# Performance work log

Measured on AMD Instinct MI355X. Metric: run time of the kernel, lower is better.

## Reference

```python
import jax, jax.numpy as jnp
import numpy as np

N_NODES = 50000
N_EDGES = 600000
IN_DIM = 128
HID = 64
HEADS = 4
NEG_SLOPE = 0.2


def _glorot(key, shape):
    fan_in, fan_out = shape[0], shape[-1]
    lim = jnp.sqrt(6.0 / (fan_in + fan_out))
    return jax.random.uniform(key, shape, jnp.float32, -lim, lim)


def setup_inputs() -> dict:
    key = jax.random.key(0)
    ks = jax.random.split(key, 16)
    x = jax.random.normal(ks[0], (N_NODES, IN_DIM), jnp.float32)
    edge_index = jax.random.randint(ks[1], (2, N_EDGES), 0, N_NODES, jnp.int32)
    # GAT layer 1: in=128 -> heads=4, out=64, concat -> 256
    W1 = _glorot(ks[2], (IN_DIM, HEADS * HID))
    a_src1 = _glorot(ks[3], (HEADS, HID))
    a_dst1 = _glorot(ks[4], (HEADS, HID))
    b1 = jnp.zeros((HEADS * HID,), jnp.float32)
    # GAT layer 2: in=256 -> heads=1, out=64, no concat
    W2 = _glorot(ks[5], (HEADS * HID, 1 * HID))
    a_src2 = _glorot(ks[6], (1, HID))
    a_dst2 = _glorot(ks[7], (1, HID))
    b2 = jnp.zeros((HID,), jnp.float32)
    # classifier: Linear(64,32) -> ReLU -> Dropout(eval: identity) -> Linear(32,2)
    Wc1 = _glorot(ks[8], (HID, 32))
    bc1 = jnp.zeros((32,), jnp.float32)
    Wc2 = _glorot(ks[9], (32, 2))
    bc2 = jnp.zeros((2,), jnp.float32)
    return {"x": x, "edge_index": edge_index,
            "W1": W1, "a_src1": a_src1, "a_dst1": a_dst1, "b1": b1,
            "W2": W2, "a_src2": a_src2, "a_dst2": a_dst2, "b2": b2,
            "Wc1": Wc1, "bc1": bc1, "Wc2": Wc2, "bc2": bc2}


def _gat_conv(x, src, dst, W, a_src, a_dst, b, heads, out_ch, concat):
    N = x.shape[0]
    h = (x @ W).reshape(N, heads, out_ch)          # [N,H,C]
    alpha_s = jnp.sum(h * a_src, axis=-1)          # [N,H]
    alpha_d = jnp.sum(h * a_dst, axis=-1)          # [N,H]
    e = jax.nn.leaky_relu(alpha_s[src] + alpha_d[dst], NEG_SLOPE)  # [E,H]
    # segment softmax over edges grouped by destination node
    m = jax.ops.segment_max(e, dst, num_segments=N)                # [N,H]
    ex = jnp.exp(e - m[dst])
    denom = jax.ops.segment_sum(ex, dst, num_segments=N)           # [N,H]
    alpha = ex / (denom[dst] + 1e-16)                              # [E,H]
    msg = h[src] * alpha[:, :, None]                               # [E,H,C]
    out = jax.ops.segment_sum(msg, dst, num_segments=N)            # [N,H,C]
    out = out.reshape(N, heads * out_ch) if concat else out.mean(axis=1)
    return out + b


def reference(x, edge_index, W1, a_src1, a_dst1, b1, W2, a_src2, a_dst2, b2,
              Wc1, bc1, Wc2, bc2):
    N = x.shape[0]
    # PyG GATConv default add_self_loops=True (same augmented edge set both layers)
    loops = jnp.arange(N, dtype=edge_index.dtype)
    src = jnp.concatenate([edge_index[0], loops])
    dst = jnp.concatenate([edge_index[1], loops])
    h = _gat_conv(x, src, dst, W1, a_src1, a_dst1, b1, HEADS, HID, True)
    h = jax.nn.relu(h)
    h = _gat_conv(h, src, dst, W2, a_src2, a_dst2, b2, 1, HID, False)
    h = jax.nn.relu(h)
    h = jax.nn.relu(h @ Wc1 + bc1)   # Dropout(0.2) is identity in eval mode
    return h @ Wc2 + bc2
```

## Files before the change

kernel.cpp:

```cpp
#include <hip/hip_runtime.h>
#include <hip/hip_fp16.h>

#define N_NODES 50000
#define N_EDGESx 600000
#define E_TOT   (N_EDGESx + N_NODES)
#define NEG_SLOPE 0.2f

typedef _Float16 f16x4 __attribute__((ext_vector_type(4)));
typedef float f32x4 __attribute__((ext_vector_type(4)));

__device__ __forceinline__ float lrelu(float x) { return x > 0.f ? x : NEG_SLOPE * x; }

__global__ __launch_bounds__(256) void count_k(const int* __restrict__ ei,
                                               int* __restrict__ counts) {
    int i = blockIdx.x * 256 + threadIdx.x;
    if (i >= E_TOT) return;
    int dst = (i < N_EDGESx) ? ei[N_EDGESx + i] : (i - N_EDGESx);
    atomicAdd(&counts[dst], 1);
}

__global__ __launch_bounds__(1024) void scanA(const int* __restrict__ counts,
                                              int* __restrict__ offs,
                                              int* __restrict__ chunks, int N) {
    __shared__ int sdata[1024];
    int t = threadIdx.x;
    int g = blockIdx.x * 1024 + t;
    int v = (g < N) ? counts[g] : 0;
    sdata[t] = v;
    __syncthreads();
    for (int off = 1; off < 1024; off <<= 1) {
        int x = (t >= off) ? sdata[t - off] : 0;
        __syncthreads();
        sdata[t] += x;
        __syncthreads();
    }
    int incl = sdata[t];
    if (g < N) offs[g] = incl - v;
    if (t == 1023) chunks[blockIdx.x] = incl;
}

__global__ void scanB(int* chunks, int nch) {
    int lane = threadIdx.x & 63;
    int orig = (lane < nch) ? chunks[lane] : 0;
    int v = orig;
#pragma unroll
    for (int off = 1; off < 64; off <<= 1) {
        int u = __shfl_up(v, off);
        if (lane >= off) v += u;
    }
    if (lane < nch) chunks[lane] = v - orig;
}

__global__ __launch_bounds__(1024) void scanC(int* __restrict__ offs,
                                              const int* __restrict__ chunks, int N) {
    int g = blockIdx.x * 1024 + threadIdx.x;
    if (g < N) offs[g] += chunks[blockIdx.x];
}

__global__ __launch_bounds__(256) void scatter_k(const int* __restrict__ ei,
                                                 const int* __restrict__ offs,
                                                 int* __restrict__ cursor,
                                                 int* __restrict__ edge_src) {
    int i = blockIdx.x * 256 + threadIdx.x;
    if (i >= E_TOT) return;
    int src, dst;
    if (i < N_EDGESx) { src = ei[i]; dst = ei[N_EDGESx + i]; }
    else              { src = dst = i - N_EDGESx; }
    int pos = atomicAdd(&cursor[dst], 1);
    edge_src[offs[dst] + pos] = src;
}

__global__ __launch_bounds__(256) void prepBoth_k(const float* __restrict__ W1,
                                                  const float* __restrict__ W2,
                                                  _Float16* __restrict__ Bt1,
                                                  _Float16* __restrict__ Bt2) {
    int b = blockIdx.x;
    if (b < 32) {
        constexpr int K = 128, N = 256;
        int q = b * 256 + threadIdx.x;
        int n = q & (N - 1);
        int k4 = q / N;
        f16x4 v;
#pragma unroll
        for (int i = 0; i < 4; ++i)
            v[i] = (_Float16)W1[(size_t)(k4 * 4 + i) * N + n];
        int idx = n * K + (((k4 >> 1) ^ (n & 15)) << 3) + ((k4 & 1) << 2);
        *(f16x4*)&Bt1[idx] = v;
    } else {
        constexpr int K = 256, N = 64;
        int q = (b - 32) * 256 + threadIdx.x;
        int n = q & (N - 1);
        int k4 = q / N;
        f16x4 v;
#pragma unroll
        for (int i = 0; i < 4; ++i) {
            int kg = k4 * 4 + i;
            int krow = (kg & 3) * 64 + (kg >> 2);
            v[i] = (_Float16)W2[(size_t)krow * N + n];
        }
        int idx = n * K + (((k4 >> 1) ^ (n & 15)) << 3) + ((k4 & 1) << 2);
        *(f16x4*)&Bt2[idx] = v;
    }
}

template<int K, int N, int CPW, typename AT, int CPERM, int ALPHA>
__global__ __launch_bounds__(256, 2) void gemm_mfma(const AT* __restrict__ A,
                                                    const _Float16* __restrict__ Bt,
                                                    _Float16* __restrict__ C,
                                                    const float* __restrict__ asrc,
                                                    const float* __restrict__ adst,
                                                    float* __restrict__ as_o,
                                                    float* __restrict__ ad_o, int M) {
    __shared__ __align__(16) _Float16 Ah[64 * K];
    __shared__ __align__(16) _Float16 Bh[N * K];
    const int t = threadIdx.x;
    const int row0 = blockIdx.x * 64;

#pragma unroll
    for (int q = t; q < 64 * K / 4; q += 256) {
        int r = q / (K / 4);
        int k4 = q % (K / 4);
        f16x4 v;
        int grow = row0 + r;
        if (grow < M) {
            if constexpr (sizeof(AT) == 4) {
                float4 f = *(const float4*)(A + (size_t)grow * K + k4 * 4);
                v[0] = (_Float16)f.x; v[1] = (_Float16)f.y;
                v[2] = (_Float16)f.z; v[3] = (_Float16)f.w;
            } else {
                v = *(const f16x4*)(A + (size_t)grow * K + k4 * 4);
            }
        } else {
            v[0] = v[1] = v[2] = v[3] = (_Float16)0.f;
        }
        int idx = r * K + (((k4 >> 1) ^ (r & 15)) << 3) + ((k4 & 1) << 2);
        *(f16x4*)&Ah[idx] = v;
    }
#pragma unroll
    for (int q = t; q < N * K / 8; q += 256)
        ((uint4*)Bh)[q] = ((const uint4*)Bt)[q];
    __syncthreads();

    const int w = t >> 6;
    const int l = t & 63;
    const int lr = l & 15;
    const int g = l >> 4;

    f32x4 acc[4][CPW];
#pragma unroll
    for (int mt = 0; mt < 4; ++mt)
#pragma unroll
        for (int nt = 0; nt < CPW; ++nt)
            acc[mt][nt] = (f32x4){0.f, 0.f, 0.f, 0.f};

#pragma unroll
    for (int ks = 0; ks < K / 16; ++ks) {
        int k = ks * 16 + g * 4;
        f16x4 a[4], b[CPW];
#pragma unroll
        for (int mt = 0; mt < 4; ++mt) {
            int r = mt * 16 + lr;
            a[mt] = *(const f16x4*)&Ah[r * K + (((k >> 3) ^ (r & 15)) << 3) + (k & 7)];
        }
#pragma unroll
        for (int nt = 0; nt < CPW; ++nt) {
            int n = (w * CPW + nt) * 16 + lr;
            b[nt] = *(const f16x4*)&Bh[n * K + (((k >> 3) ^ (n & 15)) << 3) + (k & 7)];
        }
#pragma unroll
        for (int mt = 0; mt < 4; ++mt)
#pragma unroll
            for (int nt = 0; nt < CPW; ++nt)
                acc[mt][nt] = __builtin_amdgcn_mfma_f32_16x16x16f16(a[mt], b[nt],
                                                                   acc[mt][nt], 0, 0, 0);
    }

    if constexpr (CPERM) {
        float* A_s  = (float*)Ah;
        float* A_d  = A_s + 256;
        float* psum = A_d + 256;
        __syncthreads();
        _Float16* Cs = Bh;
#pragma unroll
        for (int mt = 0; mt < 4; ++mt)
#pragma unroll
            for (int q = 0; q < 4; ++q) {
                int row = mt * 16 + g * 4 + q;
#pragma unroll
                for (int nt = 0; nt < CPW; ++nt) {
                    int gcol = (w * CPW + nt) * 16 + lr;
                    int ocol = ((gcol & 63) << 2) | (gcol >> 6);
                    Cs[row * N + ocol] = (_Float16)acc[mt][nt][q];
                }
            }
        if constexpr (ALPHA == 1) { A_s[t] = asrc[t]; A_d[t] = adst[t]; }
        __syncthreads();
#pragma unroll
        for (int q = t; q < 64 * N / 8; q += 256) {
            int row = q / (N / 8);
            int c8 = q % (N / 8);
            int grow = row0 + row;
            if (grow < M)
                *(float4*)(C + (size_t)grow * N + c8 * 8) =
                    *(const float4*)&Cs[row * N + c8 * 8];
        }
        if constexpr (ALPHA == 1) {
            int row = t & 63, qr = t >> 6;
            float s[4] = {}, d[4] = {};
#pragma unroll
            for (int j = 0; j < 16; ++j) {
                int c = qr * 16 + j;
                union { uint2 u; __half h[4]; } U;
                U.u = *(const uint2*)&Cs[row * 256 + c * 4];
#pragma unroll
                for (int h = 0; h < 4; ++h) {
                    float f = __half2float(U.h[h]);
                    s[h] += f * A_s[h * 64 + c];
                    d[h] += f * A_d[h * 64 + c];
                }
            }
            float* ps = psum + (row * 4 + qr) * 8;
#pragma unroll
            for (int h = 0; h < 4; ++h) { ps[h] = s[h]; ps[4 + h] = d[h]; }
            __syncthreads();
            if (t < 64 && row0 + t < M) {
                float4 S = make_float4(0.f, 0.f, 0.f, 0.f);
                float4 D = make_float4(0.f, 0.f, 0.f, 0.f);
#pragma unroll
                for (int q2 = 0; q2 < 4; ++q2) {
                    float* ps2 = psum + (t * 4 + q2) * 8;
                    S.x += ps2[0]; S.y += ps2[1]; S.z += ps2[2]; S.w += ps2[3];
                    D.x += ps2[4]; D.y += ps2[5]; D.z += ps2[6]; D.w += ps2[7];
                }
                *(float4*)(as_o + (size_t)(row0 + t) * 4) = S;
                *(float4*)(ad_o + (size_t)(row0 + t) * 4) = D;
            }
        }
    } else {
#pragma unroll
        for (int mt = 0; mt < 4; ++mt)
#pragma unroll
            for (int q = 0; q < 4; ++q) {
                int grow = row0 + mt * 16 + g * 4 + q;
                if (grow >= M) continue;
#pragma unroll
                for (int nt = 0; nt < CPW; ++nt) {
                    int gcol = (w * CPW + nt) * 16 + lr;
                    C[(size_t)grow * N + gcol] = (_Float16)acc[mt][nt][q];
                }
            }
        if constexpr (ALPHA == 2) {
            __half* Ch  = (__half*)Ah;
            float*  A_s = (float*)(Ch + 64 * 64);
            float*  A_d = A_s + 64;
            float*  psum = A_d + 64;
            __syncthreads();
#pragma unroll
            for (int mt = 0; mt < 4; ++mt)
#pragma unroll
                for (int q = 0; q < 4; ++q) {
                    int row = mt * 16 + g * 4 + q;
                    Ch[row * 64 + w * 16 + lr] = __float2half(acc[mt][0][q]);
                }
            if (t < 64) { A_s[t] = asrc[t]; A_d[t] = adst[t]; }
            __syncthreads();
            int row = t & 63, qr = t >> 6;
            float s = 0.f, d = 0.f;
#pragma unroll
            for (int j = 0; j < 16; ++j) {
                int c = qr * 16 + j;
                float f = __half2float(Ch[row * 64 + c]);
                s += f * A_s[c];
                d += f * A_d[c];
            }
            psum[(row * 4 + qr) * 2]     = s;
            psum[(row * 4 + qr) * 2 + 1] = d;
            __syncthreads();
            if (t < 64 && row0 + t < M) {
                float S = 0.f, D = 0.f;
#pragma unroll
                for (int q2 = 0; q2 < 4; ++q2) {
                    S += psum[(t * 4 + q2) * 2];
                    D += psum[(t * 4 + q2) * 2 + 1];
                }
                as_o[row0 + t] = S;
                ad_o[row0 + t] = D;
            }
        }
    }
}

__global__ __launch_bounds__(256) void stats1w_k(const int* __restrict__ edge_src,
                                                 const float* __restrict__ as1,
                                                 const float* __restrict__ ad1,
                                                 const int* __restrict__ offs,
                                                 const int* __restrict__ counts,
                                                 __half* __restrict__ w4, int N) {
    int lane = threadIdx.x & 63;
    int n = blockIdx.x * 4 + (threadIdx.x >> 6);
    if (n >= N) return;
    int start = offs[n];
    int end = start + counts[n];
    int h4 = lane & 3;
    float4 ad = *(const float4*)(ad1 + (size_t)n * 4);
    float adh = h4 == 0 ? ad.x : h4 == 1 ? ad.y : h4 == 2 ? ad.z : ad.w;
    float m = -1e30f, s = 0.f;
    for (int p = start + (lane >> 2); p < end; p += 16) {
        float e = lrelu(as1[(size_t)edge_src[p] * 4 + h4] + adh);
        float nm = fmaxf(m, e);
        s = s * __expf(m - nm) + __expf(e - nm);
        m = nm;
    }
#pragma unroll
    for (int i = 0; i < 4; ++i) {
        int msk = 4 << i;
        float om = __shfl_xor(m, msk);
        float os = __shfl_xor(s, msk);
        float nm = fmaxf(m, om);
        s = s * __expf(m - nm) + os * __expf(om - nm);
        m = nm;
    }
    float rcp = 1.f / (s + 1e-16f);
    float4 mh = make_float4(__shfl(m, 0), __shfl(m, 1), __shfl(m, 2), __shfl(m, 3));
    float4 rs = make_float4(__shfl(rcp, 0), __shfl(rcp, 1), __shfl(rcp, 2), __shfl(rcp, 3));
    for (int p = start + lane; p < end; p += 64) {
        float4 a = *(const float4*)(as1 + (size_t)edge_src[p] * 4);
        union { uint2 u; __half h[4]; } W;
        W.h[0] = __float2half(__expf(lrelu(a.x + ad.x) - mh.x) * rs.x);
        W.h[1] = __float2half(__expf(lrelu(a.y + ad.y) - mh.y) * rs.y);
        W.h[2] = __float2half(__expf(lrelu(a.z + ad.z) - mh.z) * rs.z);
        W.h[3] = __float2half(__expf(lrelu(a.w + ad.w) - mh.w) * rs.w);
        *(uint2*)(w4 + (size_t)p * 4) = W.u;
    }
}

__global__ __launch_bounds__(256) void stats2w_k(const int* __restrict__ edge_src,
                                                 const float* __restrict__ as2,
                                                 const float* __restrict__ ad2,
                                                 const int* __restrict__ offs,
                                                 const int* __restrict__ counts,
                                                 __half* __restrict__ w2, int N) {
    int lane = threadIdx.x & 63;
    int n = blockIdx.x * 4 + (threadIdx.x >> 6);
    if (n >= N) return;
    int start = offs[n];
    int end = start + counts[n];
    float adn = ad2[n];
    float m = -1e30f, s = 0.f;
    for (int p = start + lane; p < end; p += 64) {
        float e = lrelu(as2[edge_src[p]] + adn);
        float nm = fmaxf(m, e);
        s = s * __expf(m - nm) + __expf(e - nm);
        m = nm;
    }
#pragma unroll
    for (int i = 0; i < 6; ++i) {
        int msk = 1 << i;
        float om = __shfl_xor(m, msk);
        float os = __shfl_xor(s, msk);
        float nm = fmaxf(m, om);
        s = s * __expf(m - nm) + os * __expf(om - nm);
        m = nm;
    }
    float rn = 1.f / (s + 1e-16f);
    for (int p = start + lane; p < end; p += 64)
        w2[p] = __float2half(__expf(lrelu(as2[edge_src[p]] + adn) - m) * rn);
}

__global__ __launch_bounds__(256) void agg1_k(const __half* __restrict__ h1,
                                              const __half* __restrict__ w4,
                                              const int* __restrict__ edge_src,
                                              const int* __restrict__ offs,
                                              const int* __restrict__ counts,
                                              const float* __restrict__ b1,
                                              __half* __restrict__ out1, int N) {
    int lane = threadIdx.x & 63;
    int n = blockIdx.x * 4 + (threadIdx.x >> 6);
    if (n >= N) return;
    int start = offs[n];
    int end = start + counts[n];
    float acc0 = 0.f, acc1 = 0.f, acc2 = 0.f, acc3 = 0.f;
    int p = start;
    for (; p + 7 < end; p += 8) {
        int s[8]; uint2 hw[8], ww[8];
#pragma unroll
        for (int i = 0; i < 8; ++i) s[i] = edge_src[p + i];
#pragma unroll
        for (int i = 0; i < 8; ++i) ww[i] = *(const uint2*)(w4 + (size_t)(p + i) * 4);
#pragma unroll
        for (int i = 0; i < 8; ++i) hw[i] = *(const uint2*)(h1 + (size_t)s[i] * 256 + lane * 4);
#pragma unroll
        for (int i = 0; i < 8; ++i) {
            union { uint2 u; __half h[4]; } U, W;
            U.u = hw[i]; W.u = ww[i];
            acc0 += __half2float(U.h[0]) * __half2float(W.h[0]);
            acc1 += __half2float(U.h[1]) * __half2float(W.h[1]);
            acc2 += __half2float(U.h[2]) * __half2float(W.h[2]);
            acc3 += __half2float(U.h[3]) * __half2float(W.h[3]);
        }
    }
    for (; p + 1 < end; p += 2) {
        int s0 = edge_src[p], s1 = edge_src[p + 1];
        union { uint2 u; __half h[4]; } U0, U1, W0, W1;
        W0.u = *(const uint2*)(w4 + (size_t)p * 4);
        W1.u = *(const uint2*)(w4 + (size_t)(p + 1) * 4);
        U0.u = *(const uint2*)(h1 + (size_t)s0 * 256 + lane * 4);
        U1.u = *(const uint2*)(h1 + (size_t)s1 * 256 + lane * 4);
        acc0 += __half2float(U0.h[0]) * __half2float(W0.h[0])
              + __half2float(U1.h[0]) * __half2float(W1.h[0]);
        acc1 += __half2float(U0.h[1]) * __half2float(W0.h[1])
              + __half2float(U1.h[1]) * __half2float(W1.h[1]);
        acc2 += __half2float(U0.h[2]) * __half2float(W0.h[2])
              + __half2float(U1.h[2]) * __half2float(W1.h[2]);
        acc3 += __half2float(U0.h[3]) * __half2float(W0.h[3])
              + __half2float(U1.h[3]) * __half2float(W1.h[3]);
    }
    if (p < end) {
        int s0 = edge_src[p];
        union { uint2 u; __half h[4]; } U0, W0;
        W0.u = *(const uint2*)(w4 + (size_t)p * 4);
        U0.u = *(const uint2*)(h1 + (size_t)s0 * 256 + lane * 4);
        acc0 += __half2float(U0.h[0]) * __half2float(W0.h[0]);
        acc1 += __half2float(U0.h[1]) * __half2float(W0.h[1]);
        acc2 += __half2float(U0.h[2]) * __half2float(W0.h[2]);
        acc3 += __half2float(U0.h[3]) * __half2float(W0.h[3]);
    }
    union { uint2 u; __half h[4]; } O;
    O.h[0] = __float2half(fmaxf(acc0 + b1[lane], 0.f));
    O.h[1] = __float2half(fmaxf(acc1 + b1[64 + lane], 0.f));
    O.h[2] = __float2half(fmaxf(acc2 + b1[128 + lane], 0.f));
    O.h[3] = __float2half(fmaxf(acc3 + b1[192 + lane], 0.f));
    *(uint2*)(out1 + (size_t)n * 256 + lane * 4) = O.u;
}

__global__ __launch_bounds__(256) void agg2_k(const __half* __restrict__ h2,
                                              const __half* __restrict__ w2,
                                              const int* __restrict__ edge_src,
                                              const int* __restrict__ offs,
                                              const int* __restrict__ counts,
                                              const float* __restrict__ b2,
                                              float* __restrict__ out2, int N) {
    int l32 = threadIdx.x & 31;
    int n = blockIdx.x * 8 + (threadIdx.x >> 5);
    if (n >= N) return;
    int start = offs[n];
    int end = start + counts[n];
    float ax = 0.f, ay = 0.f;
    int p = start;
    for (; p + 7 < end; p += 8) {
        int s[8]; __half wv8[8]; __half2 hv8[8];
#pragma unroll
        for (int i = 0; i < 8; ++i) s[i] = edge_src[p + i];
#pragma unroll
        for (int i = 0; i < 8; ++i) wv8[i] = w2[p + i];
#pragma unroll
        for (int i = 0; i < 8; ++i)
            hv8[i] = *(const __half2*)(h2 + (size_t)s[i] * 64 + l32 * 2);
#pragma unroll
        for (int i = 0; i < 8; ++i) {
            float w = __half2float(wv8[i]);
            float2 f = __half22float2(hv8[i]);
            ax += f.x * w; ay += f.y * w;
        }
    }
    for (; p < end; ++p) {
        float w = __half2float(w2[p]);
        float2 f = __half22float2(*(const __half2*)(h2 + (size_t)edge_src[p] * 64 + l32 * 2));
        ax += f.x * w; ay += f.y * w;
    }
    float2 o;
    o.x = fmaxf(ax + b2[l32 * 2], 0.f);
    o.y = fmaxf(ay + b2[l32 * 2 + 1], 0.f);
    *(float2*)(out2 + (size_t)n * 64 + l32 * 2) = o;
}

__global__ __launch_bounds__(256) void cls_k(const float* __restrict__ hin,
                                             const float* __restrict__ Wc1,
                                             const float* __restrict__ bc1,
                                             const float* __restrict__ Wc2,
                                             const float* __restrict__ bc2,
                                             float* __restrict__ out, int N) {
    __shared__ float W1s[64 * 32];
    __shared__ float W2s[64];
    __shared__ float b1s[32];
    __shared__ float b2s[2];
    __shared__ float z[8][33];
    int t = threadIdx.x;
    for (int i = t; i < 2048; i += 256) W1s[i] = Wc1[i];
    if (t < 64) W2s[t] = Wc2[t];
    if (t < 32) b1s[t] = bc1[t];
    if (t < 2)  b2s[t] = bc2[t];
    __syncthreads();
    int nl = t >> 5, j = t & 31;
    int n = blockIdx.x * 8 + nl;
    float acc = b1s[j];
    if (n < N) {
        const float* hr = hin + (size_t)n * 64;
#pragma unroll 8
        for (int l = 0; l < 64; ++l) acc += hr[l] * W1s[l * 32 + j];
    }
    z[nl][j] = fmaxf(acc, 0.f);
    __syncthreads();
    if (j < 2 && n < N) {
        float o = b2s[j];
#pragma unroll
        for (int q = 0; q < 32; ++q) o += z[nl][q] * W2s[q * 2 + j];
        out[(size_t)n * 2 + j] = o;
    }
}

extern "C" void kernel_launch(void* const* d_in, const int* in_sizes, int n_in,
                              void* d_out, int out_size, void* d_ws, size_t ws_size,
                              hipStream_t stream) {
    const float* x      = (const float*)d_in[0];
    const int*   ei     = (const int*)d_in[1];
    const float* W1     = (const float*)d_in[2];
    const float* a_src1 = (const float*)d_in[3];
    const float* a_dst1 = (const float*)d_in[4];
    const float* b1     = (const float*)d_in[5];
    const float* W2     = (const float*)d_in[6];
    const float* a_src2 = (const float*)d_in[7];
    const float* a_dst2 = (const float*)d_in[8];
    const float* b2     = (const float*)d_in[9];
    const float* Wc1    = (const float*)d_in[10];
    const float* bc1    = (const float*)d_in[11];
    const float* Wc2    = (const float*)d_in[12];
    const float* bc2    = (const float*)d_in[13];

    char* ws = (char*)d_ws;
    size_t off = 0;
    auto alloc = [&](size_t bytes) -> void* {
        void* p = ws + off;
        off += (bytes + 255) & ~(size_t)255;
        return p;
    };
    int*       counts   = (int*)alloc((size_t)N_NODES * 4);
    int*       cursor   = (int*)alloc((size_t)N_NODES * 4);
    int*       offs     = (int*)alloc((size_t)N_NODES * 4);
    int*       chunks   = (int*)alloc(256);
    int*       edge_src = (int*)alloc((size_t)E_TOT * 4);
    float*     as1      = (float*)alloc((size_t)N_NODES * 16);
    float*     ad1      = (float*)alloc((size_t)N_NODES * 16);
    float*     as2      = (float*)alloc((size_t)N_NODES * 4);
    float*     ad2      = (float*)alloc((size_t)N_NODES * 4);
    __half*    w4       = (__half*)alloc((size_t)E_TOT * 8);
    _Float16*  Bt1      = (_Float16*)alloc((size_t)256 * 128 * 2);
    _Float16*  Bt2      = (_Float16*)alloc((size_t)64 * 256 * 2);
    __half*    h1h      = (__half*)alloc((size_t)N_NODES * 256 * 2);
    __half*    out1h    = (__half*)alloc((size_t)N_NODES * 256 * 2);
    float*     out2     = (float*)alloc((size_t)N_NODES * 64 * 4);
    __half*    h2h  = h1h;
    __half*    w2b  = w4;

    const int EB = (E_TOT + 255) / 256;
    const int NB4 = (N_NODES + 3) / 4;
    const int NB8 = (N_NODES + 7) / 8;
    const int NCH = (N_NODES + 1023) / 1024;
    const int MB = (N_NODES + 63) / 64;

    hipMemsetAsync(counts, 0, (size_t)N_NODES * 4, stream);
    hipMemsetAsync(cursor, 0, (size_t)N_NODES * 4, stream);

    count_k<<<EB, 256, 0, stream>>>(ei, counts);
    scanA<<<NCH, 1024, 0, stream>>>(counts, offs, chunks, N_NODES);
    scanB<<<1, 64, 0, stream>>>(chunks, NCH);
    scanC<<<NCH, 1024, 0, stream>>>(offs, chunks, N_NODES);
    scatter_k<<<EB, 256, 0, stream>>>(ei, offs, cursor, edge_src);

    prepBoth_k<<<48, 256, 0, stream>>>(W1, W2, Bt1, Bt2);

    gemm_mfma<128, 256, 4, float, 1, 1><<<MB, 256, 0, stream>>>(
        x, Bt1, (_Float16*)h1h, a_src1, a_dst1, as1, ad1, N_NODES);
    stats1w_k<<<NB4, 256, 0, stream>>>(edge_src, as1, ad1, offs, counts, w4, N_NODES);
    agg1_k<<<NB4, 256, 0, stream>>>(h1h, w4, edge_src, offs, counts, b1, out1h, N_NODES);

    gemm_mfma<256, 64, 1, _Float16, 0, 2><<<MB, 256, 0, stream>>>(
        (const _Float16*)out1h, Bt2, (_Float16*)h2h, a_src2, a_dst2, as2, ad2, N_NODES);
    stats2w_k<<<NB4, 256, 0, stream>>>(edge_src, as2, ad2, offs, counts, w2b, N_NODES);
    agg2_k<<<NB8, 256, 0, stream>>>(h2h, w2b, edge_src, offs, counts, b2, out2, N_NODES);

    cls_k<<<N_NODES / 8, 256, 0, stream>>>(out2, Wc1, bc1, Wc2, bc2, (float*)d_out, N_NODES);
}
```

Measured before the change: 261.5 us.

## Fuse layer-2 softmax stats into aggregation and add nontemporal memory hints

Removes the separate stats2w kernel and computes the layer-2 segment softmax max/sum inside the aggregation kernel. Each 32-lane group computes edge weights on the fly and broadcasts them with shuffles instead of reading a stored fp16 weight array. Streaming loads and stores in stats1, agg1 and agg2 now use nontemporal builtins. The two memsets are merged into one, assuming counts and cursor are allocated contiguously. Costs: the layer-2 attention terms are recomputed per edge, and the edge list is read several times.

```diff
diff --git a/kernel.cpp b/kernel.cpp
--- a/kernel.cpp
+++ b/kernel.cpp
@@ -8,6 +8,7 @@
 
 typedef _Float16 f16x4 __attribute__((ext_vector_type(4)));
 typedef float f32x4 __attribute__((ext_vector_type(4)));
+typedef unsigned long long u64;
 
 __device__ __forceinline__ float lrelu(float x) { return x > 0.f ? x : NEG_SLOPE * x; }
 
@@ -306,7 +307,7 @@
     float adh = h4 == 0 ? ad.x : h4 == 1 ? ad.y : h4 == 2 ? ad.z : ad.w;
     float m = -1e30f, s = 0.f;
     for (int p = start + (lane >> 2); p < end; p += 16) {
-        float e = lrelu(as1[(size_t)edge_src[p] * 4 + h4] + adh);
+        float e = lrelu(as1[(size_t)__builtin_nontemporal_load(edge_src + p) * 4 + h4] + adh);
         float nm = fmaxf(m, e);
         s = s * __expf(m - nm) + __expf(e - nm);
         m = nm;
@@ -325,46 +326,13 @@
     float4 rs = make_float4(__shfl(rcp, 0), __shfl(rcp, 1), __shfl(rcp, 2), __shfl(rcp, 3));
     for (int p = start + lane; p < end; p += 64) {
         float4 a = *(const float4*)(as1 + (size_t)edge_src[p] * 4);
-        union { uint2 u; __half h[4]; } W;
+        union { u64 u; __half h[4]; } W;
         W.h[0] = __float2half(__expf(lrelu(a.x + ad.x) - mh.x) * rs.x);
         W.h[1] = __float2half(__expf(lrelu(a.y + ad.y) - mh.y) * rs.y);
         W.h[2] = __float2half(__expf(lrelu(a.z + ad.z) - mh.z) * rs.z);
         W.h[3] = __float2half(__expf(lrelu(a.w + ad.w) - mh.w) * rs.w);
-        *(uint2*)(w4 + (size_t)p * 4) = W.u;
-    }
-}
-
-__global__ __launch_bounds__(256) void stats2w_k(const int* __restrict__ edge_src,
-                                                 const float* __restrict__ as2,
-                                                 const float* __restrict__ ad2,
-                                                 const int* __restrict__ offs,
-                                                 const int* __restrict__ counts,
-                                                 __half* __restrict__ w2, int N) {
-    int lane = threadIdx.x & 63;
-    int n = blockIdx.x * 4 + (threadIdx.x >> 6);
-    if (n >= N) return;
-    int start = offs[n];
-    int end = start + counts[n];
-    float adn = ad2[n];
-    float m = -1e30f, s = 0.f;
-    for (int p = start + lane; p < end; p += 64) {
-        float e = lrelu(as2[edge_src[p]] + adn);
-        float nm = fmaxf(m, e);
-        s = s * __expf(m - nm) + __expf(e - nm);
-        m = nm;
-    }
-#pragma unroll
-    for (int i = 0; i < 6; ++i) {
-        int msk = 1 << i;
-        float om = __shfl_xor(m, msk);
-        float os = __shfl_xor(s, msk);
-        float nm = fmaxf(m, om);
-        s = s * __expf(m - nm) + os * __expf(om - nm);
-        m = nm;
-    }
-    float rn = 1.f / (s + 1e-16f);
-    for (int p = start + lane; p < end; p += 64)
-        w2[p] = __float2half(__expf(lrelu(as2[edge_src[p]] + adn) - m) * rn);
+        __builtin_nontemporal_store(W.u, (u64*)(w4 + (size_t)p * 4));
+    }
 }
 
 __global__ __launch_bounds__(256) void agg1_k(const __half* __restrict__ h1,
@@ -382,16 +350,17 @@
     float acc0 = 0.f, acc1 = 0.f, acc2 = 0.f, acc3 = 0.f;
     int p = start;
     for (; p + 7 < end; p += 8) {
-        int s[8]; uint2 hw[8], ww[8];
-#pragma unroll
-        for (int i = 0; i < 8; ++i) s[i] = edge_src[p + i];
-#pragma unroll
-        for (int i = 0; i < 8; ++i) ww[i] = *(const uint2*)(w4 + (size_t)(p + i) * 4);
+        int s[8]; u64 ww[8]; uint2 hw[8];
+#pragma unroll
+        for (int i = 0; i < 8; ++i) s[i] = __builtin_nontemporal_load(edge_src + p + i);
+#pragma unroll
+        for (int i = 0; i < 8; ++i) ww[i] = __builtin_nontemporal_load((const u64*)(w4 + (size_t)(p + i) * 4));
 #pragma unroll
         for (int i = 0; i < 8; ++i) hw[i] = *(const uint2*)(h1 + (size_t)s[i] * 256 + lane * 4);
 #pragma unroll
         for (int i = 0; i < 8; ++i) {
-            union { uint2 u; __half h[4]; } U, W;
+            union { uint2 u; __half h[4]; } U;
+            union { u64 u; __half h[4]; } W;
             U.u = hw[i]; W.u = ww[i];
             acc0 += __half2float(U.h[0]) * __half2float(W.h[0]);
             acc1 += __half2float(U.h[1]) * __half2float(W.h[1]);
@@ -399,79 +368,86 @@
             acc3 += __half2float(U.h[3]) * __half2float(W.h[3]);
         }
     }
-    for (; p + 1 < end; p += 2) {
-        int s0 = edge_src[p], s1 = edge_src[p + 1];
-        union { uint2 u; __half h[4]; } U0, U1, W0, W1;
-        W0.u = *(const uint2*)(w4 + (size_t)p * 4);
-        W1.u = *(const uint2*)(w4 + (size_t)(p + 1) * 4);
-        U0.u = *(const uint2*)(h1 + (size_t)s0 * 256 + lane * 4);
-        U1.u = *(const uint2*)(h1 + (size_t)s1 * 256 + lane * 4);
-        acc0 += __half2float(U0.h[0]) * __half2float(W0.h[0])
-              + __half2float(U1.h[0]) * __half2float(W1.h[0]);
-        acc1 += __half2float(U0.h[1]) * __half2float(W0.h[1])
-              + __half2float(U1.h[1]) * __half2float(W1.h[1]);
-        acc2 += __half2float(U0.h[2]) * __half2float(W0.h[2])
-              + __half2float(U1.h[2]) * __half2float(W1.h[2]);
-        acc3 += __half2float(U0.h[3]) * __half2float(W0.h[3])
-              + __half2float(U1.h[3]) * __half2float(W1.h[3]);
-    }
-    if (p < end) {
+    for (; p < end; ++p) {
         int s0 = edge_src[p];
-        union { uint2 u; __half h[4]; } U0, W0;
-        W0.u = *(const uint2*)(w4 + (size_t)p * 4);
+        union { uint2 u; __half h[4]; } U0;
+        union { u64 u; __half h[4]; } W0;
+        W0.u = *(const u64*)(w4 + (size_t)p * 4);
         U0.u = *(const uint2*)(h1 + (size_t)s0 * 256 + lane * 4);
         acc0 += __half2float(U0.h[0]) * __half2float(W0.h[0]);
         acc1 += __half2float(U0.h[1]) * __half2float(W0.h[1]);
         acc2 += __half2float(U0.h[2]) * __half2float(W0.h[2]);
         acc3 += __half2float(U0.h[3]) * __half2float(W0.h[3]);
     }
-    union { uint2 u; __half h[4]; } O;
+    union { u64 u; __half h[4]; } O;
     O.h[0] = __float2half(fmaxf(acc0 + b1[lane], 0.f));
     O.h[1] = __float2half(fmaxf(acc1 + b1[64 + lane], 0.f));
     O.h[2] = __float2half(fmaxf(acc2 + b1[128 + lane], 0.f));
     O.h[3] = __float2half(fmaxf(acc3 + b1[192 + lane], 0.f));
-    *(uint2*)(out1 + (size_t)n * 256 + lane * 4) = O.u;
-}
-
-__global__ __launch_bounds__(256) void agg2_k(const __half* __restrict__ h2,
-                                              const __half* __restrict__ w2,
-                                              const int* __restrict__ edge_src,
-                                              const int* __restrict__ offs,
-                                              const int* __restrict__ counts,
-                                              const float* __restrict__ b2,
-                                              float* __restrict__ out2, int N) {
+    __builtin_nontemporal_store(O.u, (u64*)(out1 + (size_t)n * 256 + lane * 4));
+}
+
+__global__ __launch_bounds__(256) void agg2f_k(const __half* __restrict__ h2,
+                                               const float* __restrict__ as2,
+                                               const float* __restrict__ ad2,
+                                               const int* __restrict__ edge_src,
+                                               const int* __restrict__ offs,
+                                               const int* __restrict__ counts,
+                                               const float* __restrict__ b2,
+                                               float* __restrict__ out2, int N) {
+    int wl = threadIdx.x & 63;
     int l32 = threadIdx.x & 31;
     int n = blockIdx.x * 8 + (threadIdx.x >> 5);
     if (n >= N) return;
     int start = offs[n];
     int end = start + counts[n];
+    float adn = ad2[n];
+    float m = -1e30f, s = 0.f;
+    for (int p = start + l32; p < end; p += 32) {
+        float e = lrelu(as2[edge_src[p]] + adn);
+        float nm = fmaxf(m, e);
+        s = s * __expf(m - nm) + __expf(e - nm);
+        m = nm;
+    }
+#pragma unroll
+    for (int i = 0; i < 5; ++i) {
+        int msk = 1 << i;
+        float om = __shfl_xor(m, msk);
+        float os = __shfl_xor(s, msk);
+        float nm = fmaxf(m, om);
+        s = s * __expf(m - nm) + os * __expf(om - nm);
+        m = nm;
+    }
+    float rn = 1.f / (s + 1e-16f);
+    int base = wl & 32;
     float ax = 0.f, ay = 0.f;
     int p = start;
     for (; p + 7 < end; p += 8) {
-        int s[8]; __half wv8[8]; __half2 hv8[8];
-#pragma unroll
-        for (int i = 0; i < 8; ++i) s[i] = edge_src[p + i];
-#pragma unroll
-        for (int i = 0; i < 8; ++i) wv8[i] = w2[p + i];
+        int se = __builtin_nontemporal_load(edge_src + p + (l32 & 7));
+        float wv = __expf(lrelu(as2[se] + adn) - m) * rn;
+        int sidx[8]; __half2 hv8[8];
+#pragma unroll
+        for (int i = 0; i < 8; ++i) sidx[i] = edge_src[p + i];
 #pragma unroll
         for (int i = 0; i < 8; ++i)
-            hv8[i] = *(const __half2*)(h2 + (size_t)s[i] * 64 + l32 * 2);
+            hv8[i] = *(const __half2*)(h2 + (size_t)sidx[i] * 64 + l32 * 2);
 #pragma unroll
         for (int i = 0; i < 8; ++i) {
-            float w = __half2float(wv8[i]);
+            float w = __shfl(wv, base + i);
             float2 f = __half22float2(hv8[i]);
             ax += f.x * w; ay += f.y * w;
         }
     }
     for (; p < end; ++p) {
-        float w = __half2float(w2[p]);
-        float2 f = __half22float2(*(const __half2*)(h2 + (size_t)edge_src[p] * 64 + l32 * 2));
+        int s0 = edge_src[p];
+        float w = __expf(lrelu(as2[s0] + adn) - m) * rn;
+        float2 f = __half22float2(*(const __half2*)(h2 + (size_t)s0 * 64 + l32 * 2));
         ax += f.x * w; ay += f.y * w;
     }
-    float2 o;
-    o.x = fmaxf(ax + b2[l32 * 2], 0.f);
-    o.y = fmaxf(ay + b2[l32 * 2 + 1], 0.f);
-    *(float2*)(out2 + (size_t)n * 64 + l32 * 2) = o;
+    union { double d; float2 f; } O;
+    O.f.x = fmaxf(ax + b2[l32 * 2], 0.f);
+    O.f.y = fmaxf(ay + b2[l32 * 2 + 1], 0.f);
+    __builtin_nontemporal_store(O.d, (double*)(out2 + (size_t)n * 64 + l32 * 2));
 }
 
 __global__ __launch_bounds__(256) void cls_k(const float* __restrict__ hin,
@@ -550,7 +526,6 @@
     __half*    out1h    = (__half*)alloc((size_t)N_NODES * 256 * 2);
     float*     out2     = (float*)alloc((size_t)N_NODES * 64 * 4);
     __half*    h2h  = h1h;
-    __half*    w2b  = w4;
 
     const int EB = (E_TOT + 255) / 256;
     const int NB4 = (N_NODES + 3) / 4;
@@ -558,8 +533,7 @@
     const int NCH = (N_NODES + 1023) / 1024;
     const int MB = (N_NODES + 63) / 64;
 
-    hipMemsetAsync(counts, 0, (size_t)N_NODES * 4, stream);
-    hipMemsetAsync(cursor, 0, (size_t)N_NODES * 4, stream);
+    hipMemsetAsync(counts, 0, (char*)cursor - (char*)counts + (size_t)N_NODES * 4, stream);
 
     count_k<<<EB, 256, 0, stream>>>(ei, counts);
     scanA<<<NCH, 1024, 0, stream>>>(counts, offs, chunks, N_NODES);
@@ -576,8 +550,7 @@
 
     gemm_mfma<256, 64, 1, _Float16, 0, 2><<<MB, 256, 0, stream>>>(
         (const _Float16*)out1h, Bt2, (_Float16*)h2h, a_src2, a_dst2, as2, ad2, N_NODES);
-    stats2w_k<<<NB4, 256, 0, stream>>>(edge_src, as2, ad2, offs, counts, w2b, N_NODES);
-    agg2_k<<<NB8, 256, 0, stream>>>(h2h, w2b, edge_src, offs, counts, b2, out2, N_NODES);
+    agg2f_k<<<NB8, 256, 0, stream>>>(h2h, as2, ad2, edge_src, offs, counts, b2, out2, N_NODES);
 
     cls_k<<<N_NODES / 8, 256, 0, stream>>>(out2, Wc1, bc1, Wc2, bc2, (float*)d_out, N_NODES);
 }
```

Result: slower. 277.9 us (+6.3%).
